# Performance work log

Hardware: AMD Instinct MI355X
Metric: run time of the kernel (lower is better)

The kernel has to match this reference:

```python
import jax, jax.numpy as jnp
import numpy as np

B, S, E, H, BS = 4, 4096, 1024, 1024, 128  # batch, seq, embed, head_size, block_size


def setup_inputs() -> dict:
    key = jax.random.key(0)
    k1, k2, k3, k4 = jax.random.split(key, 4)
    x = jax.random.normal(k1, (B, S, E), dtype=jnp.float32)
    W_qkv = jax.random.normal(k2, (E, 3 * H), dtype=jnp.float32) * (E ** -0.5)
    W_out = jax.random.normal(k3, (H, H), dtype=jnp.float32) * (H ** -0.5)
    b_out = jax.random.normal(k4, (H,), dtype=jnp.float32) * 0.01
    return {"x": x, "W_qkv": W_qkv, "W_out": W_out, "b_out": b_out}


def reference(x, W_qkv, W_out, b_out):
    b, s, e = x.shape
    h = W_out.shape[1]
    nb = s // BS  # number of blocks (block-diagonal attention)
    qkv = x @ W_qkv                      # [B, S, 3H]
    q, k, v = jnp.split(qkv, 3, axis=-1)

    def blk(t):
        return t.reshape(b, nb, BS, h)   # [B, nb, BS, H]

    scale = h ** -0.5
    # each query block attends only its own key/value block
    scores = jnp.einsum('bnqd,bnkd->bnqk', blk(q), blk(k)) * scale  # [B, nb, BS, BS]
    causal = jnp.tril(jnp.ones((BS, BS), dtype=bool))  # diagonal block of full tril
    scores = jnp.where(causal, scores, -jnp.inf)
    scores = scores - jnp.max(scores, axis=-1, keepdims=True)
    p = jnp.exp(scores)
    p = p / (jnp.sum(p, axis=-1, keepdims=True) + 1e-6)  # faithful: softmax with +1e-6 eps
    out = jnp.einsum('bnqk,bnkd->bnqd', p, blk(v)).reshape(b, s, h)
    return out @ W_out.T + b_out
```

## Files before the change

### kernel.cpp

```cpp
#include <hip/hip_runtime.h>
#include <hip/hip_bf16.h>

typedef __attribute__((ext_vector_type(8))) short short8;
typedef __attribute__((ext_vector_type(4))) float float4_;

typedef const __attribute__((address_space(1))) void* gas_t;
typedef __attribute__((address_space(3))) void* las_t;

__device__ __forceinline__ void gl_lds16(const void* g, void* l) {
  __builtin_amdgcn_global_load_lds((gas_t)g, (las_t)l, 16, 0, 0);
}

__device__ __forceinline__ short f2b(float f) {
  union { __hip_bfloat16 h; short s; } u;
  u.h = __float2bfloat16(f);
  return u.s;
}
__device__ __forceinline__ float b2f(short s) {
  union { short s; __hip_bfloat16 h; } u;
  u.s = s;
  return __bfloat162float(u.h);
}
__device__ __forceinline__ short8 cvt8(float4_ lo, float4_ hi) {
  short8 r;
#pragma unroll
  for (int t = 0; t < 4; t++) { r[t] = f2b(lo[t]); r[t + 4] = f2b(hi[t]); }
  return r;
}

__global__ __launch_bounds__(256) void f32_to_b16(
    const float* __restrict__ in, short* __restrict__ out, long n)
{
  const long i = ((long)blockIdx.x * 256 + threadIdx.x) * 8;
  if (i >= n) return;
  float4_ lo = *(const float4_*)&in[i];
  float4_ hi = *(const float4_*)&in[i + 4];
  *(short8*)&out[i] = cvt8(lo, hi);
}

__global__ __launch_bounds__(256) void transpose64(
    const float* __restrict__ in, short* __restrict__ out, int R, int C)
{
  __shared__ __align__(16) short T[64 * 72];
  const int tid = threadIdx.x;
  const int r0 = blockIdx.y * 64;
  const int c0 = blockIdx.x * 64;
  const int r  = tid >> 2;
  const int cp = (tid & 3) * 16;
#pragma unroll
  for (int g = 0; g < 4; g++) {
    float4_ v = *(const float4_*)&in[(long)(r0 + r) * C + c0 + cp + g * 4];
#pragma unroll
    for (int t = 0; t < 4; t++) T[(cp + g * 4 + t) * 72 + r] = f2b(v[t]);
  }
  __syncthreads();
  const int c  = tid >> 2;
  const int rp = (tid & 3) * 16;
  short8 w0 = *(const short8*)&T[c * 72 + rp];
  short8 w1 = *(const short8*)&T[c * 72 + rp + 8];
  *(short8*)&out[(long)(c0 + c) * R + r0 + rp] = w0;
  *(short8*)&out[(long)(c0 + c) * R + r0 + rp + 8] = w1;
}

__global__ __launch_bounds__(256) void gemm_bt(
    const void* __restrict__ Av, int lda, int a_f32,
    const short* __restrict__ B,
    void* __restrict__ Cv, int ldc, int c_f32,
    int K, const float* __restrict__ bias)
{
  __shared__ __align__(16) short smem[2 * 128 * 32];
  const int tid  = threadIdx.x;
  const int lane = tid & 63;
  const int w    = tid >> 6;
  const int quad = lane >> 4;
  const int l15  = lane & 15;
  const int wm   = (w >> 1) * 64;
  const int wn   = (w & 1) * 64;
  const int m0   = blockIdx.y * 128;
  const int n0   = blockIdx.x * 128;
  const int wbase = w * 512;

  float4_ acc[4][4] = {};

  const int srow = tid >> 2;
  const int kp   = (tid & 3) * 8;

  for (int k0 = 0; k0 < K; k0 += 32) {
    short8 a_lo, a_hi;
    if (a_f32) {
      const float* Af = (const float*)Av;
      float4_ l0 = *(const float4_*)&Af[(long)(m0 + srow) * lda + k0 + kp];
      float4_ l1 = *(const float4_*)&Af[(long)(m0 + srow) * lda + k0 + kp + 4];
      float4_ h0 = *(const float4_*)&Af[(long)(m0 + srow + 64) * lda + k0 + kp];
      float4_ h1 = *(const float4_*)&Af[(long)(m0 + srow + 64) * lda + k0 + kp + 4];
      a_lo = cvt8(l0, l1);
      a_hi = cvt8(h0, h1);
    }
    __syncthreads();
    if (a_f32) {
      *(short8*)&smem[srow * 32 + kp]        = a_lo;
      *(short8*)&smem[(srow + 64) * 32 + kp] = a_hi;
    } else {
      const short* Ab = (const short*)Av;
      gl_lds16(&Ab[(long)(m0 + srow) * lda + k0 + kp],      &smem[wbase]);
      gl_lds16(&Ab[(long)(m0 + srow + 64) * lda + k0 + kp], &smem[2048 + wbase]);
    }
    gl_lds16(&B[(long)(n0 + srow) * K + k0 + kp],      &smem[4096 + wbase]);
    gl_lds16(&B[(long)(n0 + srow + 64) * K + k0 + kp], &smem[6144 + wbase]);
    __syncthreads();
    short8 a[4], b[4];
#pragma unroll
    for (int i = 0; i < 4; i++)
      a[i] = *(const short8*)&smem[(wm + i * 16 + l15) * 32 + quad * 8];
#pragma unroll
    for (int j = 0; j < 4; j++)
      b[j] = *(const short8*)&smem[4096 + (wn + j * 16 + l15) * 32 + quad * 8];
#pragma unroll
    for (int i = 0; i < 4; i++)
#pragma unroll
      for (int j = 0; j < 4; j++)
        acc[i][j] = __builtin_amdgcn_mfma_f32_16x16x32_bf16(a[i], b[j], acc[i][j], 0, 0, 0);
  }

  const int gidx = w >> 1;
  for (int i = 0; i < 4; i++) {
    __syncthreads();
    if (c_f32) {
      float* scr = (float*)smem;
#pragma unroll
      for (int j = 0; j < 4; j++) {
        const int col = wn + j * 16 + l15;
        const float bv = bias ? bias[n0 + col] : 0.0f;
#pragma unroll
        for (int r = 0; r < 4; r++) {
          const int row = gidx * 16 + quad * 4 + r;
          scr[row * 128 + (col ^ ((row & 7) << 4))] = acc[i][j][r] + bv;
        }
      }
    } else {
#pragma unroll
      for (int j = 0; j < 4; j++) {
        const int col = wn + j * 16 + l15;
#pragma unroll
        for (int r = 0; r < 4; r++) {
          const int row = gidx * 16 + quad * 4 + r;
          smem[row * 128 + (col ^ ((row & 7) << 4))] = f2b(acc[i][j][r]);
        }
      }
    }
    __syncthreads();
    const int rs   = tid >> 3;
    const int colp = (tid & 7) * 16;
    const int cs   = colp ^ ((rs & 7) << 4);
    const long row_g = m0 + (rs >> 4) * 64 + i * 16 + (rs & 15);
    if (c_f32) {
      float* C = (float*)Cv;
      const float* scr = (const float*)smem;
#pragma unroll
      for (int q = 0; q < 4; q++) {
        float4_ v = *(const float4_*)&scr[rs * 128 + cs + q * 4];
        *(float4_*)&C[row_g * ldc + n0 + colp + q * 4] = v;
      }
    } else {
      short* C = (short*)Cv;
      short8 v0 = *(const short8*)&smem[rs * 128 + cs];
      short8 v1 = *(const short8*)&smem[rs * 128 + cs + 8];
      *(short8*)&C[row_g * ldc + n0 + colp]     = v0;
      *(short8*)&C[row_g * ldc + n0 + colp + 8] = v1;
    }
  }
}

template<int NJ>
__device__ __forceinline__ void attn_body(short* __restrict__ qkv, int tile,
                                          short* smem)
{
  constexpr int NK    = NJ * 16;
  constexpr int STR   = NK + 8;
  constexpr int QROW0 = (NJ == 8) ? 64 : 0;
  short* Qs = smem;
  short* Ks = smem + 2048;
  short* Ps = Ks + NK * 32;
  short* Vt = Ps + 64 * STR;
  short* Ot = Vt + 64 * STR;

  const int tid  = threadIdx.x;
  const int lane = tid & 63;
  const int w    = tid >> 6;
  const int quad = lane >> 4;
  const int l15  = lane & 15;
  const long base = (long)tile * 128 * 3072;
  const int wbase = w * 512;

  const short* Qg = qkv + base + (long)QROW0 * 3072;
  const short* Kg = qkv + base + 1024;
  const short* Vg = qkv + base + 2048;

  float4_ acc[NJ] = {};
  const int srow = tid >> 2;
  const int kp   = (tid & 3) * 8;

  for (int k0 = 0; k0 < 1024; k0 += 32) {
    __syncthreads();
    gl_lds16(&Qg[(long)srow * 3072 + k0 + kp], &Qs[wbase]);
    gl_lds16(&Kg[(long)srow * 3072 + k0 + kp], &Ks[wbase]);
    if (NJ == 8)
      gl_lds16(&Kg[(long)(srow + 64) * 3072 + k0 + kp], &Ks[2048 + wbase]);
    __syncthreads();
    short8 a = *(const short8*)&Qs[(w * 16 + l15) * 32 + quad * 8];
#pragma unroll
    for (int j = 0; j < NJ; j++) {
      short8 b = *(const short8*)&Ks[(j * 16 + l15) * 32 + quad * 8];
      acc[j] = __builtin_amdgcn_mfma_f32_16x16x32_bf16(a, b, acc[j], 0, 0, 0);
    }
  }

  const float scale = 0.03125f;
#pragma unroll
  for (int r = 0; r < 4; r++) {
    const int rowq = w * 16 + quad * 4 + r;
    float s[NJ];
    float mx = -3.0e38f;
#pragma unroll
    for (int j = 0; j < NJ; j++) {
      const int col = j * 16 + l15;
      const float v = acc[j][r] * scale;
      s[j] = (col <= QROW0 + rowq) ? v : -3.0e38f;
      mx = fmaxf(mx, s[j]);
    }
    mx = fmaxf(mx, __shfl_xor(mx, 1));
    mx = fmaxf(mx, __shfl_xor(mx, 2));
    mx = fmaxf(mx, __shfl_xor(mx, 4));
    mx = fmaxf(mx, __shfl_xor(mx, 8));
    float p[NJ];
    float sum = 0.0f;
#pragma unroll
    for (int j = 0; j < NJ; j++) {
      p[j] = (s[j] > -1.0e38f) ? __expf(s[j] - mx) : 0.0f;
      sum += p[j];
    }
    sum += __shfl_xor(sum, 1);
    sum += __shfl_xor(sum, 2);
    sum += __shfl_xor(sum, 4);
    sum += __shfl_xor(sum, 8);
    const float inv = 1.0f / (sum + 1e-6f);
#pragma unroll
    for (int j = 0; j < NJ; j++)
      Ps[rowq * STR + j * 16 + l15] = f2b(p[j] * inv);
  }

  short* Op = qkv + base + (long)QROW0 * 3072;
  for (int d0 = 0; d0 < 1024; d0 += 64) {
    __syncthreads();
    if (NJ == 8) {
      const int kr = tid >> 1, dp = (tid & 1) * 32;
#pragma unroll
      for (int gg = 0; gg < 4; gg++) {
        short8 v = *(const short8*)&Vg[(long)kr * 3072 + d0 + dp + gg * 8];
#pragma unroll
        for (int t = 0; t < 8; t++) Vt[(dp + gg * 8 + t) * STR + kr] = v[t];
      }
    } else {
      const int kr = tid >> 2, dp = (tid & 3) * 16;
#pragma unroll
      for (int gg = 0; gg < 2; gg++) {
        short8 v = *(const short8*)&Vg[(long)kr * 3072 + d0 + dp + gg * 8];
#pragma unroll
        for (int t = 0; t < 8; t++) Vt[(dp + gg * 8 + t) * STR + kr] = v[t];
      }
    }
    __syncthreads();
    float4_ o[4] = {};
#pragma unroll
    for (int kk = 0; kk < NK / 32; kk++) {
      short8 a = *(const short8*)&Ps[(w * 16 + l15) * STR + kk * 32 + quad * 8];
#pragma unroll
      for (int j = 0; j < 4; j++) {
        short8 b = *(const short8*)&Vt[(j * 16 + l15) * STR + kk * 32 + quad * 8];
        o[j] = __builtin_amdgcn_mfma_f32_16x16x32_bf16(a, b, o[j], 0, 0, 0);
      }
    }
#pragma unroll
    for (int j = 0; j < 4; j++)
#pragma unroll
      for (int r = 0; r < 4; r++)
        Ot[(w * 16 + quad * 4 + r) * 72 + j * 16 + l15] = f2b(o[j][r]);
    __syncthreads();
    const int orow = tid >> 2, ocp = (tid & 3) * 16;
    short8 v0 = *(const short8*)&Ot[orow * 72 + ocp];
    short8 v1 = *(const short8*)&Ot[orow * 72 + ocp + 8];
    *(short8*)&Op[(long)orow * 3072 + d0 + ocp]     = v0;
    *(short8*)&Op[(long)orow * 3072 + d0 + ocp + 8] = v1;
  }
}

__global__ __launch_bounds__(256) void attn_blockdiag(short* __restrict__ qkv)
{
  __shared__ __align__(16) short smem[28160];
  const int tile = blockIdx.x >> 1;
  if (blockIdx.x & 1) attn_body<8>(qkv, tile, smem);
  else                attn_body<4>(qkv, tile, smem);
}

extern "C" void kernel_launch(void* const* d_in, const int* in_sizes, int n_in,
                              void* d_out, int out_size, void* d_ws, size_t ws_size,
                              hipStream_t stream) {
  const float* x    = (const float*)d_in[0];
  const float* Wqkv = (const float*)d_in[1];
  const float* Wout = (const float*)d_in[2];
  const float* bout = (const float*)d_in[3];
  float* out = (float*)d_out;

  char* ws = (char*)d_ws;
  short* WqkvT = (short*)ws;
  short* Woutb = (short*)(ws + 6291456);
  short* qkv   = (short*)(ws + 8388608);
  short* xb    = (short*)(ws + 8388608 + (size_t)16384 * 3072 * 2);

  transpose64<<<dim3(48, 16), 256, 0, stream>>>(Wqkv, WqkvT, 1024, 3072);
  f32_to_b16<<<512, 256, 0, stream>>>(Wout, Woutb, 1048576L);

  if (ws_size >= 8388608 + (size_t)16384 * 3072 * 2 + (size_t)16384 * 1024 * 2) {
    f32_to_b16<<<8192, 256, 0, stream>>>(x, xb, 16777216L);
    gemm_bt<<<dim3(24, 128), 256, 0, stream>>>(xb, 1024, 0, WqkvT,
                                               qkv, 3072, 0, 1024, nullptr);
    attn_blockdiag<<<dim3(256), 256, 0, stream>>>(qkv);
    gemm_bt<<<dim3(8, 128), 256, 0, stream>>>(qkv, 3072, 0, Woutb,
                                              out, 1024, 1, 1024, bout);
  } else if (ws_size >= 8388608 + (size_t)16384 * 3072 * 2) {
    gemm_bt<<<dim3(24, 128), 256, 0, stream>>>(x, 1024, 1, WqkvT,
                                               qkv, 3072, 0, 1024, nullptr);
    attn_blockdiag<<<dim3(256), 256, 0, stream>>>(qkv);
    gemm_bt<<<dim3(8, 128), 256, 0, stream>>>(qkv, 3072, 0, Woutb,
                                              out, 1024, 1, 1024, bout);
  } else {
    for (int c = 0; c < 4; c++) {
      const float* xc = x + (long)c * 4096 * 1024;
      float* outc = out + (long)c * 4096 * 1024;
      gemm_bt<<<dim3(24, 32), 256, 0, stream>>>(xc, 1024, 1, WqkvT,
                                                qkv, 3072, 0, 1024, nullptr);
      attn_blockdiag<<<dim3(64), 256, 0, stream>>>(qkv);
      gemm_bt<<<dim3(8, 32), 256, 0, stream>>>(qkv, 3072, 0, Woutb,
                                               outc, 1024, 1, 1024, bout);
    }
  }
}
```

Before: 376.6 us.

## Deepen GEMM K-tile to 64 with XOR-swizzled LDS, remap workgroups, fuse prep kernels

The GEMM now stages a K depth of 64 per iteration instead of 32, with XOR-swizzled LDS layouts for A and B. This halves the number of barrier pairs per K loop and aims to avoid LDS bank conflicts. Workgroup IDs are remapped into eight interleaved groups, which changes the tile visit order and may affect cache locality across the device. The three conversion and transpose launches are merged into one prep kernel to cut launch overhead, at the cost of twice the LDS per GEMM block and possibly lower occupancy.

```diff
diff --git a/kernel.cpp b/kernel.cpp
--- a/kernel.cpp
+++ b/kernel.cpp
@@ -16,11 +16,6 @@
   u.h = __float2bfloat16(f);
   return u.s;
 }
-__device__ __forceinline__ float b2f(short s) {
-  union { short s; __hip_bfloat16 h; } u;
-  u.s = s;
-  return __bfloat162float(u.h);
-}
 __device__ __forceinline__ short8 cvt8(float4_ lo, float4_ hi) {
   short8 r;
 #pragma unroll
@@ -28,38 +23,44 @@
   return r;
 }
 
-__global__ __launch_bounds__(256) void f32_to_b16(
-    const float* __restrict__ in, short* __restrict__ out, long n)
-{
-  const long i = ((long)blockIdx.x * 256 + threadIdx.x) * 8;
-  if (i >= n) return;
-  float4_ lo = *(const float4_*)&in[i];
-  float4_ hi = *(const float4_*)&in[i + 4];
-  *(short8*)&out[i] = cvt8(lo, hi);
-}
-
-__global__ __launch_bounds__(256) void transpose64(
-    const float* __restrict__ in, short* __restrict__ out, int R, int C)
+__global__ __launch_bounds__(256) void prep(
+    const float* __restrict__ Wqkv, short* __restrict__ WqkvT,
+    const float* __restrict__ Wout, short* __restrict__ Woutb,
+    const float* __restrict__ x, short* __restrict__ xb, int has_x)
 {
   __shared__ __align__(16) short T[64 * 72];
+  const int b   = blockIdx.x;
   const int tid = threadIdx.x;
-  const int r0 = blockIdx.y * 64;
-  const int c0 = blockIdx.x * 64;
-  const int r  = tid >> 2;
-  const int cp = (tid & 3) * 16;
-#pragma unroll
-  for (int g = 0; g < 4; g++) {
-    float4_ v = *(const float4_*)&in[(long)(r0 + r) * C + c0 + cp + g * 4];
-#pragma unroll
-    for (int t = 0; t < 4; t++) T[(cp + g * 4 + t) * 72 + r] = f2b(v[t]);
-  }
-  __syncthreads();
-  const int c  = tid >> 2;
-  const int rp = (tid & 3) * 16;
-  short8 w0 = *(const short8*)&T[c * 72 + rp];
-  short8 w1 = *(const short8*)&T[c * 72 + rp + 8];
-  *(short8*)&out[(long)(c0 + c) * R + r0 + rp] = w0;
-  *(short8*)&out[(long)(c0 + c) * R + r0 + rp + 8] = w1;
+  if (b < 768) {
+    const int R = 1024, C = 3072;
+    const int r0 = (b / 48) * 64;
+    const int c0 = (b % 48) * 64;
+    const int r  = tid >> 2;
+    const int cp = (tid & 3) * 16;
+#pragma unroll
+    for (int g = 0; g < 4; g++) {
+      float4_ v = *(const float4_*)&Wqkv[(long)(r0 + r) * C + c0 + cp + g * 4];
+#pragma unroll
+      for (int t = 0; t < 4; t++) T[(cp + g * 4 + t) * 72 + r] = f2b(v[t]);
+    }
+    __syncthreads();
+    const int c  = tid >> 2;
+    const int rp = (tid & 3) * 16;
+    short8 w0 = *(const short8*)&T[c * 72 + rp];
+    short8 w1 = *(const short8*)&T[c * 72 + rp + 8];
+    *(short8*)&WqkvT[(long)(c0 + c) * R + r0 + rp] = w0;
+    *(short8*)&WqkvT[(long)(c0 + c) * R + r0 + rp + 8] = w1;
+  } else if (b < 1280) {
+    const long i = ((long)(b - 768) * 256 + tid) * 8;
+    float4_ lo = *(const float4_*)&Wout[i];
+    float4_ hi = *(const float4_*)&Wout[i + 4];
+    *(short8*)&Woutb[i] = cvt8(lo, hi);
+  } else if (has_x) {
+    const long i = ((long)(b - 1280) * 256 + tid) * 8;
+    float4_ lo = *(const float4_*)&x[i];
+    float4_ hi = *(const float4_*)&x[i + 4];
+    *(short8*)&xb[i] = cvt8(lo, hi);
+  }
 }
 
 __global__ __launch_bounds__(256) void gemm_bt(
@@ -68,7 +69,8 @@
     void* __restrict__ Cv, int ldc, int c_f32,
     int K, const float* __restrict__ bias)
 {
-  __shared__ __align__(16) short smem[2 * 128 * 32];
+  __shared__ __align__(16) short As[128 * 64];
+  __shared__ __align__(16) short Bs[128 * 64];
   const int tid  = threadIdx.x;
   const int lane = tid & 63;
   const int w    = tid >> 6;
@@ -76,57 +78,81 @@
   const int l15  = lane & 15;
   const int wm   = (w >> 1) * 64;
   const int wn   = (w & 1) * 64;
-  const int m0   = blockIdx.y * 128;
-  const int n0   = blockIdx.x * 128;
+
+  const int nx  = gridDim.x;
+  const int nwg = nx * gridDim.y;
+  int wid = blockIdx.y * nx + blockIdx.x;
+  if ((nwg & 7) == 0) wid = (wid & 7) * (nwg >> 3) + (wid >> 3);
+  const int m0 = (wid / nx) * 128;
+  const int n0 = (wid % nx) * 128;
+
+  float4_ acc[4][4] = {};
+
+  const int srow = tid >> 3;
+  const int sk   = tid & 7;
+  const int kswz = ((sk ^ (srow & 7)) * 8);
   const int wbase = w * 512;
-
-  float4_ acc[4][4] = {};
-
-  const int srow = tid >> 2;
-  const int kp   = (tid & 3) * 8;
-
-  for (int k0 = 0; k0 < K; k0 += 32) {
-    short8 a_lo, a_hi;
+  const int frow = tid >> 1;
+  const int fh   = tid & 1;
+  const int swzc = quad ^ (l15 & 7);
+
+  for (int k0 = 0; k0 < K; k0 += 64) {
+    short8 fs[4];
     if (a_f32) {
       const float* Af = (const float*)Av;
-      float4_ l0 = *(const float4_*)&Af[(long)(m0 + srow) * lda + k0 + kp];
-      float4_ l1 = *(const float4_*)&Af[(long)(m0 + srow) * lda + k0 + kp + 4];
-      float4_ h0 = *(const float4_*)&Af[(long)(m0 + srow + 64) * lda + k0 + kp];
-      float4_ h1 = *(const float4_*)&Af[(long)(m0 + srow + 64) * lda + k0 + kp + 4];
-      a_lo = cvt8(l0, l1);
-      a_hi = cvt8(h0, h1);
+#pragma unroll
+      for (int g = 0; g < 2; g++) {
+        float4_ v0 = *(const float4_*)&Af[(long)(m0 + frow) * lda + k0 + fh * 32 + g * 16];
+        float4_ v1 = *(const float4_*)&Af[(long)(m0 + frow) * lda + k0 + fh * 32 + g * 16 + 4];
+        float4_ v2 = *(const float4_*)&Af[(long)(m0 + frow) * lda + k0 + fh * 32 + g * 16 + 8];
+        float4_ v3 = *(const float4_*)&Af[(long)(m0 + frow) * lda + k0 + fh * 32 + g * 16 + 12];
+        fs[g * 2]     = cvt8(v0, v1);
+        fs[g * 2 + 1] = cvt8(v2, v3);
+      }
     }
     __syncthreads();
     if (a_f32) {
-      *(short8*)&smem[srow * 32 + kp]        = a_lo;
-      *(short8*)&smem[(srow + 64) * 32 + kp] = a_hi;
+#pragma unroll
+      for (int g = 0; g < 4; g++) {
+        const int c_log = fh * 4 + g;
+        *(short8*)&As[frow * 64 + ((c_log ^ (frow & 7)) * 8)] = fs[g];
+      }
     } else {
       const short* Ab = (const short*)Av;
-      gl_lds16(&Ab[(long)(m0 + srow) * lda + k0 + kp],      &smem[wbase]);
-      gl_lds16(&Ab[(long)(m0 + srow + 64) * lda + k0 + kp], &smem[2048 + wbase]);
-    }
-    gl_lds16(&B[(long)(n0 + srow) * K + k0 + kp],      &smem[4096 + wbase]);
-    gl_lds16(&B[(long)(n0 + srow + 64) * K + k0 + kp], &smem[6144 + wbase]);
-    __syncthreads();
-    short8 a[4], b[4];
-#pragma unroll
-    for (int i = 0; i < 4; i++)
-      a[i] = *(const short8*)&smem[(wm + i * 16 + l15) * 32 + quad * 8];
-#pragma unroll
-    for (int j = 0; j < 4; j++)
-      b[j] = *(const short8*)&smem[4096 + (wn + j * 16 + l15) * 32 + quad * 8];
-#pragma unroll
-    for (int i = 0; i < 4; i++)
+#pragma unroll
+      for (int g = 0; g < 4; g++)
+        gl_lds16(&Ab[(long)(m0 + g * 32 + srow) * lda + k0 + kswz],
+                 &As[g * 2048 + wbase]);
+    }
+#pragma unroll
+    for (int g = 0; g < 4; g++)
+      gl_lds16(&B[(long)(n0 + g * 32 + srow) * K + k0 + kswz],
+               &Bs[g * 2048 + wbase]);
+    __syncthreads();
+#pragma unroll
+    for (int kk = 0; kk < 2; kk++) {
+      short8 a[4], b[4];
+      const int ch = (kk * 4) ^ swzc;
+#pragma unroll
+      for (int i = 0; i < 4; i++)
+        a[i] = *(const short8*)&As[(wm + i * 16 + l15) * 64 + ((kk * 4 + quad) ^ (l15 & 7)) * 8];
 #pragma unroll
       for (int j = 0; j < 4; j++)
-        acc[i][j] = __builtin_amdgcn_mfma_f32_16x16x32_bf16(a[i], b[j], acc[i][j], 0, 0, 0);
+        b[j] = *(const short8*)&Bs[(wn + j * 16 + l15) * 64 + ((kk * 4 + quad) ^ (l15 & 7)) * 8];
+      (void)ch;
+#pragma unroll
+      for (int i = 0; i < 4; i++)
+#pragma unroll
+        for (int j = 0; j < 4; j++)
+          acc[i][j] = __builtin_amdgcn_mfma_f32_16x16x32_bf16(a[i], b[j], acc[i][j], 0, 0, 0);
+    }
   }
 
   const int gidx = w >> 1;
   for (int i = 0; i < 4; i++) {
     __syncthreads();
     if (c_f32) {
-      float* scr = (float*)smem;
+      float* scr = (float*)As;
 #pragma unroll
       for (int j = 0; j < 4; j++) {
         const int col = wn + j * 16 + l15;
@@ -144,7 +170,7 @@
 #pragma unroll
         for (int r = 0; r < 4; r++) {
           const int row = gidx * 16 + quad * 4 + r;
-          smem[row * 128 + (col ^ ((row & 7) << 4))] = f2b(acc[i][j][r]);
+          As[row * 128 + (col ^ ((row & 7) << 4))] = f2b(acc[i][j][r]);
         }
       }
     }
@@ -155,7 +181,7 @@
     const long row_g = m0 + (rs >> 4) * 64 + i * 16 + (rs & 15);
     if (c_f32) {
       float* C = (float*)Cv;
-      const float* scr = (const float*)smem;
+      const float* scr = (const float*)As;
 #pragma unroll
       for (int q = 0; q < 4; q++) {
         float4_ v = *(const float4_*)&scr[rs * 128 + cs + q * 4];
@@ -163,8 +189,8 @@
       }
     } else {
       short* C = (short*)Cv;
-      short8 v0 = *(const short8*)&smem[rs * 128 + cs];
-      short8 v1 = *(const short8*)&smem[rs * 128 + cs + 8];
+      short8 v0 = *(const short8*)&As[rs * 128 + cs];
+      short8 v1 = *(const short8*)&As[rs * 128 + cs + 8];
       *(short8*)&C[row_g * ldc + n0 + colp]     = v0;
       *(short8*)&C[row_g * ldc + n0 + colp + 8] = v1;
     }
@@ -317,23 +343,22 @@
   short* qkv   = (short*)(ws + 8388608);
   short* xb    = (short*)(ws + 8388608 + (size_t)16384 * 3072 * 2);
 
-  transpose64<<<dim3(48, 16), 256, 0, stream>>>(Wqkv, WqkvT, 1024, 3072);
-  f32_to_b16<<<512, 256, 0, stream>>>(Wout, Woutb, 1048576L);
-
   if (ws_size >= 8388608 + (size_t)16384 * 3072 * 2 + (size_t)16384 * 1024 * 2) {
-    f32_to_b16<<<8192, 256, 0, stream>>>(x, xb, 16777216L);
+    prep<<<9472, 256, 0, stream>>>(Wqkv, WqkvT, Wout, Woutb, x, xb, 1);
     gemm_bt<<<dim3(24, 128), 256, 0, stream>>>(xb, 1024, 0, WqkvT,
                                                qkv, 3072, 0, 1024, nullptr);
     attn_blockdiag<<<dim3(256), 256, 0, stream>>>(qkv);
     gemm_bt<<<dim3(8, 128), 256, 0, stream>>>(qkv, 3072, 0, Woutb,
                                               out, 1024, 1, 1024, bout);
   } else if (ws_size >= 8388608 + (size_t)16384 * 3072 * 2) {
+    prep<<<1280, 256, 0, stream>>>(Wqkv, WqkvT, Wout, Woutb, nullptr, nullptr, 0);
     gemm_bt<<<dim3(24, 128), 256, 0, stream>>>(x, 1024, 1, WqkvT,
                                                qkv, 3072, 0, 1024, nullptr);
     attn_blockdiag<<<dim3(256), 256, 0, stream>>>(qkv);
     gemm_bt<<<dim3(8, 128), 256, 0, stream>>>(qkv, 3072, 0, Woutb,
                                               out, 1024, 1, 1024, bout);
   } else {
+    prep<<<1280, 256, 0, stream>>>(Wqkv, WqkvT, Wout, Woutb, nullptr, nullptr, 0);
     for (int c = 0; c < 4; c++) {
       const float* xc = x + (long)c * 4096 * 1024;
       float* outc = out + (long)c * 4096 * 1024;
```

After: 345.9 us. 1.09x faster.
